# Kernel optimization log

Measured on AMD Instinct MI355X. Metric: run time of the kernel, lower is better.

The kernel has to match this reference:

```python
import jax, jax.numpy as jnp
import numpy as np

PI = float(np.pi)


def _layernorm(x, g, b, eps=1e-5):
    mu = jnp.mean(x, axis=-1, keepdims=True)
    var = jnp.var(x, axis=-1, keepdims=True)
    return (x - mu) * jax.lax.rsqrt(var + eps) * g + b


def setup_inputs() -> dict:
    key = jax.random.key(0)
    B, L, D, P = 4, 2048, 256, 32
    ks = jax.random.split(key, 16)

    def lin_w(k, fi, fo):
        return (jax.random.normal(k, (fi, fo), dtype=jnp.float32) / np.sqrt(fi)).astype(jnp.float32)

    inp = {
        'x': jax.random.normal(ks[0], (B, L, D), dtype=jnp.float32),
        'pos_phases': jax.random.normal(ks[1], (L, P), dtype=jnp.float32) * PI,
        'w_mem1v': lin_w(ks[2], D, P), 'b_mem1v': jnp.zeros((P,), jnp.float32),
        'w_mem1o': lin_w(ks[3], P, D), 'b_mem1o': jnp.zeros((D,), jnp.float32),
        'w_off': lin_w(ks[4], D + P, P), 'b_off': jnp.zeros((P,), jnp.float32),
        'w_key': lin_w(ks[5], D, P), 'b_key': jnp.zeros((P,), jnp.float32),
        'w_val': lin_w(ks[6], D, D), 'b_val': jnp.zeros((D,), jnp.float32),
        'w_sk1': lin_w(ks[7], 2 * D, D), 'b_sk1': jnp.zeros((D,), jnp.float32),
        'w_sk2': lin_w(ks[8], D, P), 'b_sk2': jnp.zeros((P,), jnp.float32),
        'w_gate': lin_w(ks[9], D, 1), 'b_gate': jnp.zeros((1,), jnp.float32),
        'ln_g': jnp.ones((D,), jnp.float32), 'ln_b': jnp.zeros((D,), jnp.float32),
        'w_out': lin_w(ks[10], D, D), 'b_out': jnp.zeros((D,), jnp.float32),
    }
    return inp


def reference(x, pos_phases, w_mem1v, b_mem1v, w_mem1o, b_mem1o, w_off, b_off,
              w_key, b_key, w_val, b_val, w_sk1, b_sk1, w_sk2, b_sk2,
              w_gate, b_gate, ln_g, ln_b, w_out, b_out):
    B, L, D = x.shape
    P = pos_phases.shape[-1]

    pos_cos = jnp.cos(pos_phases)  # [L,P]
    pos_sin = jnp.sin(pos_phases)

    # Memory 1: flat [B,L,P] phasor cumulative memory
    v1 = x @ w_mem1v + b_mem1v                       # [B,L,P]
    mem1_cos = jnp.cumsum(pos_cos[None] * v1, axis=1)
    mem1_sin = jnp.cumsum(pos_sin[None] * v1, axis=1)

    offset_input = jnp.concatenate([x, jnp.broadcast_to(pos_phases[None], (B, L, P))], axis=-1)
    offset = jnp.tanh(offset_input @ w_off + b_off) * PI
    oc, os = jnp.cos(offset), jnp.sin(offset)
    query_cos = pos_cos[None] * oc - pos_sin[None] * os
    query_sin = pos_sin[None] * oc + pos_cos[None] * os
    pos_ret = (mem1_cos * query_cos + mem1_sin * query_sin) / np.sqrt(P)
    pos_out = pos_ret @ w_mem1o + b_mem1o            # [B,L,D]

    # Memory 2: full [B,L,P,D] phasor KV cumulative memory
    key_phases = jnp.tanh(x @ w_key + b_key) * PI    # [B,L,P]
    key_cos, key_sin = jnp.cos(key_phases), jnp.sin(key_phases)
    values = x @ w_val + b_val                       # [B,L,D]
    store_gate = jax.nn.sigmoid(x @ w_gate + b_gate) # [B,L,1]

    positions = jnp.arange(1, L + 1, dtype=x.dtype)[None, :, None]
    context_avg = jnp.cumsum(x, axis=1) / positions
    h = jax.nn.gelu(jnp.concatenate([x, context_avg], axis=-1) @ w_sk1 + b_sk1, approximate=False)
    storage_phases = jnp.tanh(h @ w_sk2 + b_sk2) * PI  # [B,L,P]

    gated_v = values * store_gate                    # [B,L,D]
    kv_mem_cos = jnp.cumsum(jnp.cos(storage_phases)[..., None] * gated_v[:, :, None, :], axis=1)  # [B,L,P,D]
    kv_mem_sin = jnp.cumsum(jnp.sin(storage_phases)[..., None] * gated_v[:, :, None, :], axis=1)

    gate_cumsum = jnp.clip(jnp.cumsum(store_gate, axis=1), 1.0, None)  # [B,L,1]
    kv_retrieved = jnp.einsum('blpd,blp->bld', kv_mem_cos, key_cos) + \
                   jnp.einsum('blpd,blp->bld', kv_mem_sin, key_sin)
    kv_retrieved = kv_retrieved / (jnp.sqrt(gate_cumsum) * np.sqrt(P))

    combined = pos_out + kv_retrieved
    return x + _layernorm(combined, ln_g, ln_b) @ w_out + b_out
```

## Files before the change

### kernel.cpp

```cpp
#include <hip/hip_runtime.h>
#include <hip/hip_bf16.h>

constexpr int B_ = 4;
constexpr int L_ = 2048;
constexpr int D_ = 256;
constexpr int P_ = 32;
constexpr int CL = 32;
constexpr int NC = L_ / CL;

#define PI_F 3.14159265358979323846f
#define INV_SQRT_P 0.17677669529663687f

typedef __attribute__((ext_vector_type(8))) short short8_t;
typedef __attribute__((ext_vector_type(4))) float floatx4;

static __device__ inline short f2bf(float f) {
  unsigned int u;
  __builtin_memcpy(&u, &f, 4);
  unsigned int r = (u + 0x7fffu + ((u >> 16) & 1u)) >> 16;
  return (short)r;
}
static __device__ inline float bf2f(short s) {
  unsigned int u = ((unsigned int)(unsigned short)s) << 16;
  float f;
  __builtin_memcpy(&f, &u, 4);
  return f;
}

__global__ void wprep(const float* __restrict__ x, const float* __restrict__ pos,
                      const float* __restrict__ w_val, const float* __restrict__ w_mem1v,
                      const float* __restrict__ w_off, const float* __restrict__ b_off,
                      const float* __restrict__ w_key, const float* __restrict__ w_gate,
                      const float* __restrict__ w_sk1, const float* __restrict__ w_out,
                      const float* __restrict__ w_sk2, const float* __restrict__ w_mem1o,
                      short* __restrict__ WA, short* __restrict__ W1,
                      short* __restrict__ WO, short* __restrict__ W2T,
                      short* __restrict__ W1OT,
                      short* __restrict__ xbf, float* __restrict__ poff) {
  int blk = blockIdx.x, tid = threadIdx.x;
  if (blk < 384) {
    int idx = blk * 256 + tid;
    int n = idx >> 8, k = idx & 255;
    float v;
    if (n < 256) v = w_val[k * 256 + n];
    else if (n < 288) v = w_mem1v[k * 32 + (n - 256)];
    else if (n < 320) v = w_off[k * 32 + (n - 288)];
    else if (n < 352) v = w_key[k * 32 + (n - 320)];
    else if (n == 352) v = w_gate[k];
    else v = 0.f;
    WA[idx] = f2bf(v);
  } else if (blk < 896) {
    int idx = (blk - 384) * 256 + tid;
    int n = idx >> 9, k = idx & 511;
    W1[idx] = f2bf(w_sk1[k * 256 + n]);
  } else if (blk < 1152) {
    int idx = (blk - 896) * 256 + tid;
    int n = idx >> 8, k = idx & 255;
    WO[idx] = f2bf(w_out[k * 256 + n]);
  } else if (blk < 1184) {
    int idx = (blk - 1152) * 256 + tid;
    int p = idx >> 8, k = idx & 255;
    W2T[idx] = f2bf(w_sk2[k * 32 + p]);
  } else if (blk < 1216) {
    int idx = (blk - 1184) * 256 + tid;
    int d = idx >> 5, p = idx & 31;
    W1OT[idx] = f2bf(w_mem1o[p * 256 + d]);
  } else if (blk < 3264) {
    int idx = ((blk - 1216) * 256 + tid) * 4;
    float4 v = *(const float4*)&x[idx];
    short4 o;
    o.x = f2bf(v.x); o.y = f2bf(v.y); o.z = f2bf(v.z); o.w = f2bf(v.w);
    *(short4*)&xbf[idx] = o;
  } else {
    int idx = (blk - 3264) * 256 + tid;
    int l = idx >> 5, p = idx & 31;
    float a = b_off[p];
    for (int j = 0; j < 32; ++j) a += pos[l * 32 + j] * w_off[(256 + j) * 32 + p];
    poff[idx] = a;
  }
}

template <int KTILES, int NBLK, int MODE>
__global__ __launch_bounds__(256) void gemm_k(const short* __restrict__ A0,
                                              const short* __restrict__ A1,
                                              const short* __restrict__ W,
                                              const float* __restrict__ bias,
                                              const float* __restrict__ xres,
                                              float* __restrict__ outf,
                                              short* __restrict__ outb) {
  __shared__ short As[64][136];
  __shared__ short Bs[64][136];
  int tid = threadIdx.x;
  int mg = blockIdx.x / NBLK, ng = blockIdx.x % NBLK;
  int tok0 = mg * 64, n0 = ng * 64;
  int lane = tid & 63, w = tid >> 6;
  int mw = (w & 1) * 32, nw = (w >> 1) * 32;
  floatx4 acc[2][2] = {{{0.f, 0.f, 0.f, 0.f}, {0.f, 0.f, 0.f, 0.f}},
                       {{0.f, 0.f, 0.f, 0.f}, {0.f, 0.f, 0.f, 0.f}}};
  int r2 = tid >> 4, c8 = tid & 15;
  int ml = lane & 15, kq = (lane >> 4) * 8;
  const int K = KTILES * 128;

  for (int kt = 0; kt < KTILES; ++kt) {
    const short* Asrc;
    int cb;
    if (KTILES == 4) {
      Asrc = (kt < 2) ? A0 : A1;
      cb = (kt & 1) * 128;
    } else {
      Asrc = A0;
      cb = kt * 128;
    }
#pragma unroll
    for (int pass = 0; pass < 4; ++pass) {
      int row = pass * 16 + r2;
      *(short8_t*)&As[row][c8 * 8] =
          *(const short8_t*)&Asrc[(tok0 + row) * 256 + cb + c8 * 8];
      *(short8_t*)&Bs[row][c8 * 8] =
          *(const short8_t*)&W[(n0 + row) * K + kt * 128 + c8 * 8];
    }
    __syncthreads();
#pragma unroll
    for (int s = 0; s < 4; ++s) {
      short8_t a0 = *(short8_t*)&As[mw + ml][s * 32 + kq];
      short8_t a1 = *(short8_t*)&As[mw + 16 + ml][s * 32 + kq];
      short8_t b0 = *(short8_t*)&Bs[nw + ml][s * 32 + kq];
      short8_t b1 = *(short8_t*)&Bs[nw + 16 + ml][s * 32 + kq];
      acc[0][0] = __builtin_amdgcn_mfma_f32_16x16x32_bf16(a0, b0, acc[0][0], 0, 0, 0);
      acc[0][1] = __builtin_amdgcn_mfma_f32_16x16x32_bf16(a0, b1, acc[0][1], 0, 0, 0);
      acc[1][0] = __builtin_amdgcn_mfma_f32_16x16x32_bf16(a1, b0, acc[1][0], 0, 0, 0);
      acc[1][1] = __builtin_amdgcn_mfma_f32_16x16x32_bf16(a1, b1, acc[1][1], 0, 0, 0);
    }
    __syncthreads();
  }
  int col = lane & 15, rq = (lane >> 4) * 4;
#pragma unroll
  for (int nt = 0; nt < 2; ++nt) {
    int n = n0 + nw + nt * 16 + col;
    float bv = (MODE == 0) ? 0.f : bias[n];
#pragma unroll
    for (int mt = 0; mt < 2; ++mt) {
#pragma unroll
      for (int rg = 0; rg < 4; ++rg) {
        int tok = tok0 + mw + mt * 16 + rq + rg;
        float v = acc[mt][nt][rg] + bv;
        if (MODE == 0) {
          outb[tok * 384 + n] = f2bf(v);
        } else if (MODE == 1) {
          float g = 0.5f * v * (1.f + erff(v * 0.70710678118654752f));
          outb[tok * 256 + n] = f2bf(g);
        } else {
          outf[tok * 256 + n] = xres[tok * 256 + n] + v;
        }
      }
    }
  }
}

__global__ void kernelA3(const short* __restrict__ Ybf, const float* __restrict__ pos,
                         const float* __restrict__ poff, const float* __restrict__ b_mem1v,
                         const float* __restrict__ b_key, const float* __restrict__ b_gate,
                         const float* __restrict__ b_val,
                         float* __restrict__ m1cT, float* __restrict__ m1sT,
                         float* __restrict__ qc, float* __restrict__ qs,
                         short* __restrict__ K2bf, short* __restrict__ gvT,
                         float* __restrict__ sg) {
  __shared__ float gsh[8];
  int tid = threadIdx.x;
  int tok0 = blockIdx.x * 8;
  int t = tid >> 5, p = tid & 31;
  int tok = tok0 + t, l = tok & (L_ - 1);
  int b = tok >> 11;
  float gate = 1.f / (1.f + expf(-(bf2f(Ybf[tok * 384 + 352]) + b_gate[0])));
  if (p == 0) {
    sg[tok] = gate;
    gsh[t] = gate;
  }
  float v1 = bf2f(Ybf[tok * 384 + 256 + p]) + b_mem1v[p];
  float ph = pos[l * 32 + p];
  float pc = cosf(ph), ps = sinf(ph);
  int idxT = (b * 32 + p) * L_ + l;
  m1cT[idxT] = pc * v1;
  m1sT[idxT] = ps * v1;
  float off = tanhf(bf2f(Ybf[tok * 384 + 288 + p]) + poff[l * 32 + p]) * PI_F;
  float oc = cosf(off), os = sinf(off);
  int idx = tok * 32 + p;
  qc[idx] = pc * oc - ps * os;
  qs[idx] = ps * oc + pc * os;
  float kp = tanhf(bf2f(Ybf[tok * 384 + 320 + p]) + b_key[p]) * PI_F;
  K2bf[tok * 64 + p] = f2bf(cosf(kp));
  K2bf[tok * 64 + 32 + p] = f2bf(sinf(kp));
  __syncthreads();
  {
    int l0 = tok0 & (L_ - 1);
    int bc = (tok0 >> 11) * NC + (l0 >> 5);
    int tl0 = l0 & 31;
    short sv[8];
#pragma unroll
    for (int tt = 0; tt < 8; ++tt)
      sv[tt] = f2bf((bf2f(Ybf[(tok0 + tt) * 384 + tid]) + b_val[tid]) * gsh[tt]);
    *(short8_t*)&gvT[(bc * 256 + tid) * 32 + tl0] = *(short8_t*)sv;
  }
}

__global__ void scan_all(float* __restrict__ m1cT, float* __restrict__ m1sT,
                         float* __restrict__ sg, const float* __restrict__ x,
                         float* __restrict__ ctxsum) {
  int blk = blockIdx.x;
  int tid = threadIdx.x;
  if (blk >= 260) {
    int c2 = blk - 260;
    int b = c2 >> 6, ch = c2 & 63;
    int xb = (b * L_ + ch * 32) * 256 + tid;
    float s = 0.f;
#pragma unroll 8
    for (int i = 0; i < 32; ++i) s += x[xb + i * 256];
    ctxsum[c2 * 256 + tid] = s;
    return;
  }
  int lane = tid & 63, wid = tid >> 6;
  __shared__ float wsum[4];
  float carry = 0.f;
  float* arr;
  int base;
  if (blk < 256) {
    arr = (blk < 128) ? m1cT : m1sT;
    base = (blk & 127) * L_;
  } else {
    arr = sg;
    base = (blk - 256) * L_;
  }
  for (int t0 = 0; t0 < L_; t0 += 256) {
    int l = t0 + tid;
    float v = arr[base + l];
#pragma unroll
    for (int off = 1; off < 64; off <<= 1) {
      float n = __shfl_up(v, off, 64);
      if (lane >= off) v += n;
    }
    if (lane == 63) wsum[wid] = v;
    __syncthreads();
    float add = carry;
    for (int w = 0; w < wid; ++w) add += wsum[w];
    arr[base + l] = v + add;
    carry += wsum[0] + wsum[1] + wsum[2] + wsum[3];
    __syncthreads();
  }
}

__global__ void kernelCtx(const float* __restrict__ x, const float* __restrict__ ctxsum,
                          short* __restrict__ ctxbf) {
  int c2 = blockIdx.x;
  int b = c2 >> 6, ch = c2 & 63;
  int tid = threadIdx.x;
  float run = 0.f;
  int sb = b * 64 * 256 + tid;
  for (int c = 0; c < ch; ++c) run += ctxsum[sb + c * 256];
  int xb = (b * L_ + ch * 32) * 256 + tid;
#pragma unroll 8
  for (int i = 0; i < 32; ++i) {
    run += x[xb + i * 256];
    int l = ch * 32 + i;
    ctxbf[xb + i * 256] = f2bf(run / (float)(l + 1));
  }
}

__global__ __launch_bounds__(256) void kernelCD(const short* __restrict__ hs,
                                                const short* __restrict__ W2T,
                                                const float* __restrict__ b_sk2,
                                                const short* __restrict__ gvT,
                                                short* __restrict__ SPbf,
                                                short* __restrict__ UT) {
  __shared__ __align__(16) short SPL[2][64][40];
  int tid = threadIdx.x;
  int tok0 = blockIdx.x * 64;
  int lane = tid & 63, w = tid >> 6;
  int ml = lane & 15, quad = lane >> 4, kq = quad * 8;
  int m0 = w * 16;
  floatx4 pacc[2] = {};
#pragma unroll
  for (int s = 0; s < 8; ++s) {
    short8_t a = *(const short8_t*)&hs[(tok0 + m0 + ml) * 256 + s * 32 + kq];
    short8_t b0 = *(const short8_t*)&W2T[ml * 256 + s * 32 + kq];
    short8_t b1 = *(const short8_t*)&W2T[(16 + ml) * 256 + s * 32 + kq];
    pacc[0] = __builtin_amdgcn_mfma_f32_16x16x32_bf16(a, b0, pacc[0], 0, 0, 0);
    pacc[1] = __builtin_amdgcn_mfma_f32_16x16x32_bf16(a, b1, pacc[1], 0, 0, 0);
  }
  int cl = w >> 1;
#pragma unroll
  for (int nt = 0; nt < 2; ++nt) {
    int p = nt * 16 + ml;
    float bs = b_sk2[p];
#pragma unroll
    for (int r = 0; r < 4; ++r) {
      int tok = tok0 + m0 + quad * 4 + r;
      float sp = tanhf(pacc[nt][r] + bs) * PI_F;
      short c = f2bf(cosf(sp)), s = f2bf(sinf(sp));
      int tl = (w & 1) * 16 + quad * 4 + r;
      SPL[cl][p][tl] = c;
      SPL[cl][32 + p][tl] = s;
      SPbf[tok * 64 + p] = c;
      SPbf[tok * 64 + 32 + p] = s;
    }
  }
  __syncthreads();
  int c2 = w & 1, dbase = (w >> 1) * 128;
  int bc = blockIdx.x * 2 + c2;
  short8_t a[4];
#pragma unroll
  for (int mt = 0; mt < 4; ++mt) a[mt] = *(short8_t*)&SPL[c2][mt * 16 + ml][kq];
#pragma unroll
  for (int dp = 0; dp < 2; ++dp) {
    floatx4 acc[4][4] = {};
#pragma unroll
    for (int nt = 0; nt < 4; ++nt) {
      short8_t b = *(const short8_t*)&gvT[(bc * 256 + dbase + dp * 64 + nt * 16 + ml) * 32 + kq];
#pragma unroll
      for (int mt = 0; mt < 4; ++mt)
        acc[mt][nt] = __builtin_amdgcn_mfma_f32_16x16x32_bf16(a[mt], b, acc[mt][nt], 0, 0, 0);
    }
#pragma unroll
    for (int mt = 0; mt < 4; ++mt)
#pragma unroll
      for (int nt = 0; nt < 4; ++nt)
#pragma unroll
        for (int r = 0; r < 4; ++r) {
          int q = mt * 16 + quad * 4 + r;
          int d = dbase + dp * 64 + nt * 16 + ml;
          UT[(bc * 256 + d) * 64 + q] = f2bf(acc[mt][nt][r]);
        }
  }
}

__global__ void kernelE(short* __restrict__ UT) {
  int tid = blockIdx.x * 256 + threadIdx.x;
  int q = tid & 63;
  int d = (tid >> 6) & 255;
  int b = tid >> 14;
  int base = ((b * NC) * 256 + d) * 64 + q;
  const int cs = 256 * 64;
  float run = 0.f;
  for (int c0 = 0; c0 < NC; c0 += 8) {
    short v[8];
#pragma unroll
    for (int j = 0; j < 8; ++j) v[j] = UT[base + (c0 + j) * cs];
#pragma unroll
    for (int j = 0; j < 8; ++j) {
      UT[base + (c0 + j) * cs] = f2bf(run);
      run += bf2f(v[j]);
    }
  }
}

__global__ __launch_bounds__(256) void kernelFG(const short* __restrict__ UT,
                                                const short* __restrict__ SPbf,
                                                const short* __restrict__ K2bf,
                                                const short* __restrict__ gvT,
                                                const float* __restrict__ sgc,
                                                const float* __restrict__ m1cT,
                                                const float* __restrict__ m1sT,
                                                const float* __restrict__ qc,
                                                const float* __restrict__ qs,
                                                const short* __restrict__ W1OT,
                                                const float* __restrict__ b_mem1o,
                                                const float* __restrict__ ln_g,
                                                const float* __restrict__ ln_b,
                                                short* __restrict__ cbn) {
  __shared__ __align__(16) short SL[32][40];
  __shared__ __align__(16) short PR[32][40];
  __shared__ float CMB[32][260];
  __shared__ float scl[32], mu_s[32], rs_s[32];
  int tid = threadIdx.x;
  int bc = blockIdx.x;
  int lbase = bc * CL;
  int bb = bc >> 6, lloc = (bc & 63) * 32;
  if (tid < 32) scl[tid] = rsqrtf(fmaxf(sgc[lbase + tid], 1.f)) * INV_SQRT_P;
  for (int it = 0; it < 4; ++it) {
    int i = it * 256 + tid;
    int p = i >> 5, t = i & 31;
    int gT = (bb * 32 + p) * L_ + lloc + t;
    int g = (lbase + t) * 32 + p;
    PR[t][p] = f2bf((m1cT[gT] * qc[g] + m1sT[gT] * qs[g]) * INV_SQRT_P);
  }
  int lane = tid & 63, w = tid >> 6;
  int ml = lane & 15, quad = lane >> 4, kq = quad * 8;
  floatx4 acc[2][4] = {};
  short8_t ka0 = *(const short8_t*)&K2bf[(lbase + ml) * 64 + kq];
  short8_t ka1 = *(const short8_t*)&K2bf[(lbase + 16 + ml) * 64 + kq];
  short8_t kb0 = *(const short8_t*)&K2bf[(lbase + ml) * 64 + 32 + kq];
  short8_t kb1 = *(const short8_t*)&K2bf[(lbase + 16 + ml) * 64 + 32 + kq];
#pragma unroll
  for (int nt = 0; nt < 4; ++nt) {
    short8_t b = *(const short8_t*)&UT[(bc * 256 + w * 64 + nt * 16 + ml) * 64 + kq];
    acc[0][nt] = __builtin_amdgcn_mfma_f32_16x16x32_bf16(ka0, b, acc[0][nt], 0, 0, 0);
    acc[1][nt] = __builtin_amdgcn_mfma_f32_16x16x32_bf16(ka1, b, acc[1][nt], 0, 0, 0);
  }
  if (w == 0) {
    floatx4 sacc[2][2] = {};
#pragma unroll
    for (int ks2 = 0; ks2 < 2; ++ks2) {
      short8_t a0 = (ks2 == 0) ? ka0 : kb0;
      short8_t a1 = (ks2 == 0) ? ka1 : kb1;
      short8_t b0 = *(const short8_t*)&SPbf[(lbase + ml) * 64 + ks2 * 32 + kq];
      short8_t b1 = *(const short8_t*)&SPbf[(lbase + 16 + ml) * 64 + ks2 * 32 + kq];
      sacc[0][0] = __builtin_amdgcn_mfma_f32_16x16x32_bf16(a0, b0, sacc[0][0], 0, 0, 0);
      sacc[0][1] = __builtin_amdgcn_mfma_f32_16x16x32_bf16(a0, b1, sacc[0][1], 0, 0, 0);
      sacc[1][0] = __builtin_amdgcn_mfma_f32_16x16x32_bf16(a1, b0, sacc[1][0], 0, 0, 0);
      sacc[1][1] = __builtin_amdgcn_mfma_f32_16x16x32_bf16(a1, b1, sacc[1][1], 0, 0, 0);
    }
#pragma unroll
    for (int mt = 0; mt < 2; ++mt)
#pragma unroll
      for (int nt = 0; nt < 2; ++nt)
#pragma unroll
        for (int r = 0; r < 4; ++r) {
          int trow = mt * 16 + quad * 4 + r;
          int scol = nt * 16 + ml;
          float v = (scol <= trow) ? sacc[mt][nt][r] : 0.f;
          SL[trow][scol] = f2bf(v);
        }
  }
  __syncthreads();
#pragma unroll
  for (int nt = 0; nt < 4; ++nt) {
    short8_t b = *(const short8_t*)&UT[(bc * 256 + w * 64 + nt * 16 + ml) * 64 + 32 + kq];
    acc[0][nt] = __builtin_amdgcn_mfma_f32_16x16x32_bf16(kb0, b, acc[0][nt], 0, 0, 0);
    acc[1][nt] = __builtin_amdgcn_mfma_f32_16x16x32_bf16(kb1, b, acc[1][nt], 0, 0, 0);
  }
  {
    short8_t a0 = *(short8_t*)&SL[ml][kq];
    short8_t a1 = *(short8_t*)&SL[16 + ml][kq];
#pragma unroll
    for (int nt = 0; nt < 4; ++nt) {
      short8_t b = *(const short8_t*)&gvT[(bc * 256 + w * 64 + nt * 16 + ml) * 32 + kq];
      acc[0][nt] = __builtin_amdgcn_mfma_f32_16x16x32_bf16(a0, b, acc[0][nt], 0, 0, 0);
      acc[1][nt] = __builtin_amdgcn_mfma_f32_16x16x32_bf16(a1, b, acc[1][nt], 0, 0, 0);
    }
  }
  floatx4 macc[2][4] = {};
  {
    short8_t a0 = *(short8_t*)&PR[ml][kq];
    short8_t a1 = *(short8_t*)&PR[16 + ml][kq];
#pragma unroll
    for (int nt = 0; nt < 4; ++nt) {
      short8_t b = *(const short8_t*)&W1OT[(w * 64 + nt * 16 + ml) * 32 + kq];
      macc[0][nt] = __builtin_amdgcn_mfma_f32_16x16x32_bf16(a0, b, macc[0][nt], 0, 0, 0);
      macc[1][nt] = __builtin_amdgcn_mfma_f32_16x16x32_bf16(a1, b, macc[1][nt], 0, 0, 0);
    }
  }
#pragma unroll
  for (int mt = 0; mt < 2; ++mt)
#pragma unroll
    for (int nt = 0; nt < 4; ++nt) {
      int d = w * 64 + nt * 16 + ml;
      float bm = b_mem1o[d];
#pragma unroll
      for (int r = 0; r < 4; ++r) {
        int t = mt * 16 + quad * 4 + r;
        CMB[t][d] = acc[mt][nt][r] * scl[t] + macc[mt][nt][r] + bm;
      }
    }
  __syncthreads();
  {
    int t = tid >> 3, g = tid & 7;
    float s = 0.f, s2 = 0.f;
#pragma unroll
    for (int j = 0; j < 32; ++j) {
      float v = CMB[t][g + j * 8];
      s += v;
      s2 += v * v;
    }
#pragma unroll
    for (int m = 1; m < 8; m <<= 1) {
      s += __shfl_xor(s, m, 64);
      s2 += __shfl_xor(s2, m, 64);
    }
    if (g == 0) {
      float mu = s / (float)D_;
      float var = s2 / (float)D_ - mu * mu;
      mu_s[t] = mu;
      rs_s[t] = rsqrtf(var + 1e-5f);
    }
  }
  __syncthreads();
  {
    float lg = ln_g[tid], lb = ln_b[tid];
#pragma unroll
    for (int t = 0; t < 32; ++t)
      cbn[(lbase + t) * 256 + tid] = f2bf((CMB[t][tid] - mu_s[t]) * rs_s[t] * lg + lb);
  }
}

extern "C" void kernel_launch(void* const* d_in, const int* in_sizes, int n_in,
                              void* d_out, int out_size, void* d_ws, size_t ws_size,
                              hipStream_t stream) {
  const float* x = (const float*)d_in[0];
  const float* pos = (const float*)d_in[1];
  const float* w_mem1v = (const float*)d_in[2];
  const float* b_mem1v = (const float*)d_in[3];
  const float* w_mem1o = (const float*)d_in[4];
  const float* b_mem1o = (const float*)d_in[5];
  const float* w_off = (const float*)d_in[6];
  const float* b_off = (const float*)d_in[7];
  const float* w_key = (const float*)d_in[8];
  const float* b_key = (const float*)d_in[9];
  const float* w_val = (const float*)d_in[10];
  const float* b_val = (const float*)d_in[11];
  const float* w_sk1 = (const float*)d_in[12];
  const float* b_sk1 = (const float*)d_in[13];
  const float* w_sk2 = (const float*)d_in[14];
  const float* b_sk2 = (const float*)d_in[15];
  const float* w_gate = (const float*)d_in[16];
  const float* b_gate = (const float*)d_in[17];
  const float* ln_g = (const float*)d_in[18];
  const float* ln_b = (const float*)d_in[19];
  const float* w_out = (const float*)d_in[20];
  const float* b_out = (const float*)d_in[21];
  float* out = (float*)d_out;
  float* ws = (float*)d_ws;

  const int BLP = B_ * L_ * P_;
  const int BLD = B_ * L_ * D_;
  float* m1cT = ws;
  float* m1sT = m1cT + BLP;
  float* qc = m1sT + BLP;
  float* qs = qc + BLP;
  float* sg = qs + BLP;
  float* poff = sg + B_ * L_;
  float* ctxsum = poff + L_ * P_;
  short* Ybf = (short*)(ctxsum + B_ * 64 * 256);
  short* UT = Ybf;
  short* xbf = UT + (size_t)B_ * NC * 256 * 64;
  short* cbn = xbf;
  short* ctxbf = xbf + BLD;
  short* hs = ctxbf + BLD;
  short* gvT = hs + BLD;
  short* K2bf = gvT + BLD;
  short* SPbf = K2bf + B_ * L_ * 64;
  short* WA = SPbf + B_ * L_ * 64;
  short* W1 = WA + 384 * 256;
  short* WO = W1 + 256 * 512;
  short* W2T = WO + 256 * 256;
  short* W1OT = W2T + 32 * 256;

  wprep<<<3520, 256, 0, stream>>>(x, pos, w_val, w_mem1v, w_off, b_off, w_key, w_gate,
                                  w_sk1, w_out, w_sk2, w_mem1o, WA, W1, WO, W2T, W1OT,
                                  xbf, poff);
  gemm_k<2, 6, 0><<<128 * 6, 256, 0, stream>>>(xbf, nullptr, WA, nullptr, nullptr, nullptr, Ybf);
  kernelA3<<<(B_ * L_) / 8, 256, 0, stream>>>(Ybf, pos, poff, b_mem1v, b_key, b_gate, b_val,
                                              m1cT, m1sT, qc, qs, K2bf, gvT, sg);
  scan_all<<<516, 256, 0, stream>>>(m1cT, m1sT, sg, x, ctxsum);
  kernelCtx<<<256, 256, 0, stream>>>(x, ctxsum, ctxbf);
  gemm_k<4, 4, 1><<<128 * 4, 256, 0, stream>>>(xbf, ctxbf, W1, b_sk1, nullptr, nullptr, hs);
  kernelCD<<<(B_ * L_) / 64, 256, 0, stream>>>(hs, W2T, b_sk2, gvT, SPbf, UT);
  kernelE<<<256, 256, 0, stream>>>(UT);
  kernelFG<<<B_ * NC, 256, 0, stream>>>(UT, SPbf, K2bf, gvT, sg, m1cT, m1sT, qc, qs,
                                        W1OT, b_mem1o, ln_g, ln_b, cbn);
  gemm_k<2, 4, 2><<<128 * 4, 256, 0, stream>>>(cbn, nullptr, WO, b_out, x, out, nullptr);
}
```

Baseline: 190.6 us.

## Fuse scan-stage kernels into persistent launches with software grid barriers

Merges kernelA3, scan_all and kernelCtx into one 516-block kernel, and kernelCD, kernelE and kernelFG into one 256-block kernel. The stages are separated by atomic-counter grid barriers instead of kernel boundaries. This removes several launch gaps and tail drains. It relies on every block being co-resident, which risks deadlock if occupancy is not enough, and it adds barrier latency. kernelA3 now handles 16 tokens per block instead of 8.

```diff
diff --git a/kernel.cpp b/kernel.cpp
--- a/kernel.cpp
+++ b/kernel.cpp
@@ -25,6 +25,24 @@
   float f;
   __builtin_memcpy(&f, &u, 4);
   return f;
+}
+
+static __device__ inline void gbar(unsigned* bar, unsigned nb) {
+  __syncthreads();
+  if (threadIdx.x == 0) {
+    __threadfence();
+    unsigned g = __hip_atomic_load(bar + 1, __ATOMIC_ACQUIRE, __HIP_MEMORY_SCOPE_AGENT);
+    unsigned a = __hip_atomic_fetch_add(bar, 1u, __ATOMIC_ACQ_REL, __HIP_MEMORY_SCOPE_AGENT);
+    if (a + 1 == nb) {
+      __hip_atomic_store(bar, 0u, __ATOMIC_RELAXED, __HIP_MEMORY_SCOPE_AGENT);
+      __hip_atomic_fetch_add(bar + 1, 1u, __ATOMIC_RELEASE, __HIP_MEMORY_SCOPE_AGENT);
+    } else {
+      while (__hip_atomic_load(bar + 1, __ATOMIC_ACQUIRE, __HIP_MEMORY_SCOPE_AGENT) == g)
+        __builtin_amdgcn_s_sleep(2);
+    }
+    __threadfence();
+  }
+  __syncthreads();
 }
 
 __global__ void wprep(const float* __restrict__ x, const float* __restrict__ pos,
@@ -36,8 +54,10 @@
                       short* __restrict__ WA, short* __restrict__ W1,
                       short* __restrict__ WO, short* __restrict__ W2T,
                       short* __restrict__ W1OT,
-                      short* __restrict__ xbf, float* __restrict__ poff) {
+                      short* __restrict__ xbf, float* __restrict__ poff,
+                      unsigned* __restrict__ bar) {
   int blk = blockIdx.x, tid = threadIdx.x;
+  if (blk == 0 && tid < 8) bar[tid] = 0u;
   if (blk < 384) {
     int idx = blk * 256 + tid;
     int n = idx >> 8, k = idx & 255;
@@ -157,57 +177,62 @@
   }
 }
 
-__global__ void kernelA3(const short* __restrict__ Ybf, const float* __restrict__ pos,
-                         const float* __restrict__ poff, const float* __restrict__ b_mem1v,
-                         const float* __restrict__ b_key, const float* __restrict__ b_gate,
-                         const float* __restrict__ b_val,
-                         float* __restrict__ m1cT, float* __restrict__ m1sT,
-                         float* __restrict__ qc, float* __restrict__ qs,
-                         short* __restrict__ K2bf, short* __restrict__ gvT,
-                         float* __restrict__ sg) {
-  __shared__ float gsh[8];
-  int tid = threadIdx.x;
-  int tok0 = blockIdx.x * 8;
-  int t = tid >> 5, p = tid & 31;
-  int tok = tok0 + t, l = tok & (L_ - 1);
-  int b = tok >> 11;
-  float gate = 1.f / (1.f + expf(-(bf2f(Ybf[tok * 384 + 352]) + b_gate[0])));
-  if (p == 0) {
-    sg[tok] = gate;
-    gsh[t] = gate;
-  }
-  float v1 = bf2f(Ybf[tok * 384 + 256 + p]) + b_mem1v[p];
-  float ph = pos[l * 32 + p];
-  float pc = cosf(ph), ps = sinf(ph);
-  int idxT = (b * 32 + p) * L_ + l;
-  m1cT[idxT] = pc * v1;
-  m1sT[idxT] = ps * v1;
-  float off = tanhf(bf2f(Ybf[tok * 384 + 288 + p]) + poff[l * 32 + p]) * PI_F;
-  float oc = cosf(off), os = sinf(off);
-  int idx = tok * 32 + p;
-  qc[idx] = pc * oc - ps * os;
-  qs[idx] = ps * oc + pc * os;
-  float kp = tanhf(bf2f(Ybf[tok * 384 + 320 + p]) + b_key[p]) * PI_F;
-  K2bf[tok * 64 + p] = f2bf(cosf(kp));
-  K2bf[tok * 64 + 32 + p] = f2bf(sinf(kp));
-  __syncthreads();
-  {
-    int l0 = tok0 & (L_ - 1);
-    int bc = (tok0 >> 11) * NC + (l0 >> 5);
-    int tl0 = l0 & 31;
-    short sv[8];
-#pragma unroll
-    for (int tt = 0; tt < 8; ++tt)
-      sv[tt] = f2bf((bf2f(Ybf[(tok0 + tt) * 384 + tid]) + b_val[tid]) * gsh[tt]);
-    *(short8_t*)&gvT[(bc * 256 + tid) * 32 + tl0] = *(short8_t*)sv;
-  }
-}
-
-__global__ void scan_all(float* __restrict__ m1cT, float* __restrict__ m1sT,
-                         float* __restrict__ sg, const float* __restrict__ x,
-                         float* __restrict__ ctxsum) {
-  int blk = blockIdx.x;
-  int tid = threadIdx.x;
+__global__ __launch_bounds__(256, 4) void kernelA3SC(
+    const short* __restrict__ Ybf, const float* __restrict__ pos,
+    const float* __restrict__ poff, const float* __restrict__ b_mem1v,
+    const float* __restrict__ b_key, const float* __restrict__ b_gate,
+    const float* __restrict__ b_val,
+    float* __restrict__ m1cT, float* __restrict__ m1sT,
+    float* __restrict__ qc, float* __restrict__ qs,
+    short* __restrict__ K2bf, short* __restrict__ gvT,
+    float* __restrict__ sg, const float* __restrict__ x,
+    float* __restrict__ ctxsum, short* __restrict__ ctxbf,
+    unsigned* __restrict__ bar) {
+  __shared__ float gsh[16];
+  __shared__ float wsum[4];
+  int blk = blockIdx.x, tid = threadIdx.x;
+  if (blk < 512) {
+    int tok0 = blk * 16;
+#pragma unroll
+    for (int h = 0; h < 2; ++h) {
+      int t = h * 8 + (tid >> 5), p = tid & 31;
+      int tok = tok0 + t, l = tok & (L_ - 1);
+      int b = tok >> 11;
+      float gate = 1.f / (1.f + expf(-(bf2f(Ybf[tok * 384 + 352]) + b_gate[0])));
+      if (p == 0) {
+        sg[tok] = gate;
+        gsh[t] = gate;
+      }
+      float v1 = bf2f(Ybf[tok * 384 + 256 + p]) + b_mem1v[p];
+      float ph = pos[l * 32 + p];
+      float pc = cosf(ph), ps = sinf(ph);
+      int idxT = (b * 32 + p) * L_ + l;
+      m1cT[idxT] = pc * v1;
+      m1sT[idxT] = ps * v1;
+      float off = tanhf(bf2f(Ybf[tok * 384 + 288 + p]) + poff[l * 32 + p]) * PI_F;
+      float oc = cosf(off), os = sinf(off);
+      int idx = tok * 32 + p;
+      qc[idx] = pc * oc - ps * os;
+      qs[idx] = ps * oc + pc * os;
+      float kp = tanhf(bf2f(Ybf[tok * 384 + 320 + p]) + b_key[p]) * PI_F;
+      K2bf[tok * 64 + p] = f2bf(cosf(kp));
+      K2bf[tok * 64 + 32 + p] = f2bf(sinf(kp));
+    }
+    __syncthreads();
+    {
+      int l0 = tok0 & (L_ - 1);
+      int bc = (tok0 >> 11) * NC + (l0 >> 5);
+      int tl0 = l0 & 31;
+      short sv[16];
+#pragma unroll
+      for (int tt = 0; tt < 16; ++tt)
+        sv[tt] = f2bf((bf2f(Ybf[(tok0 + tt) * 384 + tid]) + b_val[tid]) * gsh[tt]);
+      int gb = (bc * 256 + tid) * 32 + tl0;
+      *(short8_t*)&gvT[gb] = *(short8_t*)&sv[0];
+      *(short8_t*)&gvT[gb + 8] = *(short8_t*)&sv[8];
+    }
+  }
+  gbar(bar + 0, gridDim.x);
   if (blk >= 260) {
     int c2 = blk - 260;
     int b = c2 >> 6, ch = c2 & 63;
@@ -216,278 +241,270 @@
 #pragma unroll 8
     for (int i = 0; i < 32; ++i) s += x[xb + i * 256];
     ctxsum[c2 * 256 + tid] = s;
-    return;
-  }
-  int lane = tid & 63, wid = tid >> 6;
-  __shared__ float wsum[4];
-  float carry = 0.f;
-  float* arr;
-  int base;
-  if (blk < 256) {
-    arr = (blk < 128) ? m1cT : m1sT;
-    base = (blk & 127) * L_;
   } else {
-    arr = sg;
-    base = (blk - 256) * L_;
-  }
-  for (int t0 = 0; t0 < L_; t0 += 256) {
-    int l = t0 + tid;
-    float v = arr[base + l];
-#pragma unroll
-    for (int off = 1; off < 64; off <<= 1) {
-      float n = __shfl_up(v, off, 64);
-      if (lane >= off) v += n;
-    }
-    if (lane == 63) wsum[wid] = v;
-    __syncthreads();
-    float add = carry;
-    for (int w = 0; w < wid; ++w) add += wsum[w];
-    arr[base + l] = v + add;
-    carry += wsum[0] + wsum[1] + wsum[2] + wsum[3];
-    __syncthreads();
-  }
-}
-
-__global__ void kernelCtx(const float* __restrict__ x, const float* __restrict__ ctxsum,
-                          short* __restrict__ ctxbf) {
-  int c2 = blockIdx.x;
-  int b = c2 >> 6, ch = c2 & 63;
-  int tid = threadIdx.x;
-  float run = 0.f;
-  int sb = b * 64 * 256 + tid;
-  for (int c = 0; c < ch; ++c) run += ctxsum[sb + c * 256];
-  int xb = (b * L_ + ch * 32) * 256 + tid;
+    int lane = tid & 63, wid = tid >> 6;
+    float carry = 0.f;
+    float* arr;
+    int base;
+    if (blk < 256) {
+      arr = (blk < 128) ? m1cT : m1sT;
+      base = (blk & 127) * L_;
+    } else {
+      arr = sg;
+      base = (blk - 256) * L_;
+    }
+    for (int t0 = 0; t0 < L_; t0 += 256) {
+      int l = t0 + tid;
+      float v = arr[base + l];
+#pragma unroll
+      for (int off = 1; off < 64; off <<= 1) {
+        float n = __shfl_up(v, off, 64);
+        if (lane >= off) v += n;
+      }
+      if (lane == 63) wsum[wid] = v;
+      __syncthreads();
+      float add = carry;
+      for (int w = 0; w < wid; ++w) add += wsum[w];
+      arr[base + l] = v + add;
+      carry += wsum[0] + wsum[1] + wsum[2] + wsum[3];
+      __syncthreads();
+    }
+  }
+  gbar(bar + 2, gridDim.x);
+  if (blk >= 260) {
+    int c2 = blk - 260;
+    int b = c2 >> 6, ch = c2 & 63;
+    float run = 0.f;
+    int sb = b * 64 * 256 + tid;
+    for (int c = 0; c < ch; ++c) run += ctxsum[sb + c * 256];
+    int xb = (b * L_ + ch * 32) * 256 + tid;
 #pragma unroll 8
-  for (int i = 0; i < 32; ++i) {
-    run += x[xb + i * 256];
-    int l = ch * 32 + i;
-    ctxbf[xb + i * 256] = f2bf(run / (float)(l + 1));
-  }
-}
-
-__global__ __launch_bounds__(256) void kernelCD(const short* __restrict__ hs,
-                                                const short* __restrict__ W2T,
-                                                const float* __restrict__ b_sk2,
-                                                const short* __restrict__ gvT,
-                                                short* __restrict__ SPbf,
-                                                short* __restrict__ UT) {
-  __shared__ __align__(16) short SPL[2][64][40];
-  int tid = threadIdx.x;
-  int tok0 = blockIdx.x * 64;
+    for (int i = 0; i < 32; ++i) {
+      run += x[xb + i * 256];
+      int l = ch * 32 + i;
+      ctxbf[xb + i * 256] = f2bf(run / (float)(l + 1));
+    }
+  }
+}
+
+__global__ __launch_bounds__(256) void kernelKV(
+    const short* __restrict__ hs, const short* __restrict__ W2T,
+    const float* __restrict__ b_sk2, const short* __restrict__ gvT,
+    short* __restrict__ SPbf, short* __restrict__ UT,
+    const short* __restrict__ K2bf, const float* __restrict__ sgc,
+    const float* __restrict__ m1cT, const float* __restrict__ m1sT,
+    const float* __restrict__ qc, const float* __restrict__ qs,
+    const short* __restrict__ W1OT, const float* __restrict__ b_mem1o,
+    const float* __restrict__ ln_g, const float* __restrict__ ln_b,
+    short* __restrict__ cbn, unsigned* __restrict__ bar) {
+  __shared__ __align__(16) char shm[38912];
+  int blk = blockIdx.x, tid = threadIdx.x;
   int lane = tid & 63, w = tid >> 6;
   int ml = lane & 15, quad = lane >> 4, kq = quad * 8;
-  int m0 = w * 16;
-  floatx4 pacc[2] = {};
-#pragma unroll
-  for (int s = 0; s < 8; ++s) {
-    short8_t a = *(const short8_t*)&hs[(tok0 + m0 + ml) * 256 + s * 32 + kq];
-    short8_t b0 = *(const short8_t*)&W2T[ml * 256 + s * 32 + kq];
-    short8_t b1 = *(const short8_t*)&W2T[(16 + ml) * 256 + s * 32 + kq];
-    pacc[0] = __builtin_amdgcn_mfma_f32_16x16x32_bf16(a, b0, pacc[0], 0, 0, 0);
-    pacc[1] = __builtin_amdgcn_mfma_f32_16x16x32_bf16(a, b1, pacc[1], 0, 0, 0);
-  }
-  int cl = w >> 1;
-#pragma unroll
-  for (int nt = 0; nt < 2; ++nt) {
-    int p = nt * 16 + ml;
-    float bs = b_sk2[p];
-#pragma unroll
-    for (int r = 0; r < 4; ++r) {
-      int tok = tok0 + m0 + quad * 4 + r;
-      float sp = tanhf(pacc[nt][r] + bs) * PI_F;
-      short c = f2bf(cosf(sp)), s = f2bf(sinf(sp));
-      int tl = (w & 1) * 16 + quad * 4 + r;
-      SPL[cl][p][tl] = c;
-      SPL[cl][32 + p][tl] = s;
-      SPbf[tok * 64 + p] = c;
-      SPbf[tok * 64 + 32 + p] = s;
-    }
-  }
-  __syncthreads();
-  int c2 = w & 1, dbase = (w >> 1) * 128;
-  int bc = blockIdx.x * 2 + c2;
-  short8_t a[4];
-#pragma unroll
-  for (int mt = 0; mt < 4; ++mt) a[mt] = *(short8_t*)&SPL[c2][mt * 16 + ml][kq];
-#pragma unroll
-  for (int dp = 0; dp < 2; ++dp) {
-    floatx4 acc[4][4] = {};
+  if (blk < 128) {
+    short* SPL = (short*)shm;
+    int tok0 = blk * 64;
+    int m0 = w * 16;
+    floatx4 pacc[2] = {};
+#pragma unroll
+    for (int s = 0; s < 8; ++s) {
+      short8_t a = *(const short8_t*)&hs[(tok0 + m0 + ml) * 256 + s * 32 + kq];
+      short8_t b0 = *(const short8_t*)&W2T[ml * 256 + s * 32 + kq];
+      short8_t b1 = *(const short8_t*)&W2T[(16 + ml) * 256 + s * 32 + kq];
+      pacc[0] = __builtin_amdgcn_mfma_f32_16x16x32_bf16(a, b0, pacc[0], 0, 0, 0);
+      pacc[1] = __builtin_amdgcn_mfma_f32_16x16x32_bf16(a, b1, pacc[1], 0, 0, 0);
+    }
+    int cl = w >> 1;
+#pragma unroll
+    for (int nt = 0; nt < 2; ++nt) {
+      int p = nt * 16 + ml;
+      float bs = b_sk2[p];
+#pragma unroll
+      for (int r = 0; r < 4; ++r) {
+        int tok = tok0 + m0 + quad * 4 + r;
+        float sp = tanhf(pacc[nt][r] + bs) * PI_F;
+        short c = f2bf(cosf(sp)), s = f2bf(sinf(sp));
+        int tl = (w & 1) * 16 + quad * 4 + r;
+        SPL[(cl * 64 + p) * 40 + tl] = c;
+        SPL[(cl * 64 + 32 + p) * 40 + tl] = s;
+        SPbf[tok * 64 + p] = c;
+        SPbf[tok * 64 + 32 + p] = s;
+      }
+    }
+    __syncthreads();
+    int c2 = w & 1, dbase = (w >> 1) * 128;
+    int bc = blk * 2 + c2;
+    short8_t a[4];
+#pragma unroll
+    for (int mt = 0; mt < 4; ++mt)
+      a[mt] = *(short8_t*)&SPL[(c2 * 64 + mt * 16 + ml) * 40 + kq];
+#pragma unroll
+    for (int dp = 0; dp < 2; ++dp) {
+      floatx4 acc[4][4] = {};
+#pragma unroll
+      for (int nt = 0; nt < 4; ++nt) {
+        short8_t b = *(const short8_t*)&gvT[(bc * 256 + dbase + dp * 64 + nt * 16 + ml) * 32 + kq];
+#pragma unroll
+        for (int mt = 0; mt < 4; ++mt)
+          acc[mt][nt] = __builtin_amdgcn_mfma_f32_16x16x32_bf16(a[mt], b, acc[mt][nt], 0, 0, 0);
+      }
+#pragma unroll
+      for (int mt = 0; mt < 4; ++mt)
+#pragma unroll
+        for (int nt = 0; nt < 4; ++nt)
+#pragma unroll
+          for (int r = 0; r < 4; ++r) {
+            int q = mt * 16 + quad * 4 + r;
+            int d = dbase + dp * 64 + nt * 16 + ml;
+            UT[(bc * 256 + d) * 64 + q] = f2bf(acc[mt][nt][r]);
+          }
+    }
+  }
+  gbar(bar + 4, gridDim.x);
+  {
+    int gt = blk * 256 + tid;
+    int q = gt & 63;
+    int d = (gt >> 6) & 255;
+    int b = gt >> 14;
+    int base = ((b * NC) * 256 + d) * 64 + q;
+    const int cs = 256 * 64;
+    float run = 0.f;
+    for (int c0 = 0; c0 < NC; c0 += 8) {
+      short v[8];
+#pragma unroll
+      for (int j = 0; j < 8; ++j) v[j] = UT[base + (c0 + j) * cs];
+#pragma unroll
+      for (int j = 0; j < 8; ++j) {
+        UT[base + (c0 + j) * cs] = f2bf(run);
+        run += bf2f(v[j]);
+      }
+    }
+  }
+  gbar(bar + 6, gridDim.x);
+  {
+    short* SL = (short*)shm;
+    short* PR = SL + 32 * 40;
+    float* CMB = (float*)(shm + 5120);
+    float* scl = (float*)(shm + 5120 + 33280);
+    float* mu_s = scl + 32;
+    float* rs_s = scl + 64;
+    int bc = blk;
+    int lbase = bc * CL;
+    int bb = bc >> 6, lloc = (bc & 63) * 32;
+    if (tid < 32) scl[tid] = rsqrtf(fmaxf(sgc[lbase + tid], 1.f)) * INV_SQRT_P;
+    for (int it = 0; it < 4; ++it) {
+      int i = it * 256 + tid;
+      int p = i >> 5, t = i & 31;
+      int gT = (bb * 32 + p) * L_ + lloc + t;
+      int g = (lbase + t) * 32 + p;
+      PR[t * 40 + p] = f2bf((m1cT[gT] * qc[g] + m1sT[gT] * qs[g]) * INV_SQRT_P);
+    }
+    floatx4 acc[2][4] = {};
+    short8_t ka0 = *(const short8_t*)&K2bf[(lbase + ml) * 64 + kq];
+    short8_t ka1 = *(const short8_t*)&K2bf[(lbase + 16 + ml) * 64 + kq];
+    short8_t kb0 = *(const short8_t*)&K2bf[(lbase + ml) * 64 + 32 + kq];
+    short8_t kb1 = *(const short8_t*)&K2bf[(lbase + 16 + ml) * 64 + 32 + kq];
 #pragma unroll
     for (int nt = 0; nt < 4; ++nt) {
-      short8_t b = *(const short8_t*)&gvT[(bc * 256 + dbase + dp * 64 + nt * 16 + ml) * 32 + kq];
-#pragma unroll
-      for (int mt = 0; mt < 4; ++mt)
-        acc[mt][nt] = __builtin_amdgcn_mfma_f32_16x16x32_bf16(a[mt], b, acc[mt][nt], 0, 0, 0);
-    }
-#pragma unroll
-    for (int mt = 0; mt < 4; ++mt)
-#pragma unroll
-      for (int nt = 0; nt < 4; ++nt)
+      short8_t b = *(const short8_t*)&UT[(bc * 256 + w * 64 + nt * 16 + ml) * 64 + kq];
+      acc[0][nt] = __builtin_amdgcn_mfma_f32_16x16x32_bf16(ka0, b, acc[0][nt], 0, 0, 0);
+      acc[1][nt] = __builtin_amdgcn_mfma_f32_16x16x32_bf16(ka1, b, acc[1][nt], 0, 0, 0);
+    }
+    if (w == 0) {
+      floatx4 sacc[2][2] = {};
+#pragma unroll
+      for (int ks2 = 0; ks2 < 2; ++ks2) {
+        short8_t a0 = (ks2 == 0) ? ka0 : kb0;
+        short8_t a1 = (ks2 == 0) ? ka1 : kb1;
+        short8_t b0 = *(const short8_t*)&SPbf[(lbase + ml) * 64 + ks2 * 32 + kq];
+        short8_t b1 = *(const short8_t*)&SPbf[(lbase + 16 + ml) * 64 + ks2 * 32 + kq];
+        sacc[0][0] = __builtin_amdgcn_mfma_f32_16x16x32_bf16(a0, b0, sacc[0][0], 0, 0, 0);
+        sacc[0][1] = __builtin_amdgcn_mfma_f32_16x16x32_bf16(a0, b1, sacc[0][1], 0, 0, 0);
+        sacc[1][0] = __builtin_amdgcn_mfma_f32_16x16x32_bf16(a1, b0, sacc[1][0], 0, 0, 0);
+        sacc[1][1] = __builtin_amdgcn_mfma_f32_16x16x32_bf16(a1, b1, sacc[1][1], 0, 0, 0);
+      }
+#pragma unroll
+      for (int mt = 0; mt < 2; ++mt)
+#pragma unroll
+        for (int nt = 0; nt < 2; ++nt)
+#pragma unroll
+          for (int r = 0; r < 4; ++r) {
+            int trow = mt * 16 + quad * 4 + r;
+            int scol = nt * 16 + ml;
+            float v = (scol <= trow) ? sacc[mt][nt][r] : 0.f;
+            SL[trow * 40 + scol] = f2bf(v);
+          }
+    }
+    __syncthreads();
+#pragma unroll
+    for (int nt = 0; nt < 4; ++nt) {
+      short8_t b = *(const short8_t*)&UT[(bc * 256 + w * 64 + nt * 16 + ml) * 64 + 32 + kq];
+      acc[0][nt] = __builtin_amdgcn_mfma_f32_16x16x32_bf16(kb0, b, acc[0][nt], 0, 0, 0);
+      acc[1][nt] = __builtin_amdgcn_mfma_f32_16x16x32_bf16(kb1, b, acc[1][nt], 0, 0, 0);
+    }
+    {
+      short8_t a0 = *(short8_t*)&SL[ml * 40 + kq];
+      short8_t a1 = *(short8_t*)&SL[(16 + ml) * 40 + kq];
+#pragma unroll
+      for (int nt = 0; nt < 4; ++nt) {
+        short8_t b = *(const short8_t*)&gvT[(bc * 256 + w * 64 + nt * 16 + ml) * 32 + kq];
+        acc[0][nt] = __builtin_amdgcn_mfma_f32_16x16x32_bf16(a0, b, acc[0][nt], 0, 0, 0);
+        acc[1][nt] = __builtin_amdgcn_mfma_f32_16x16x32_bf16(a1, b, acc[1][nt], 0, 0, 0);
+      }
+    }
+    floatx4 macc[2][4] = {};
+    {
+      short8_t a0 = *(short8_t*)&PR[ml * 40 + kq];
+      short8_t a1 = *(short8_t*)&PR[(16 + ml) * 40 + kq];
+#pragma unroll
+      for (int nt = 0; nt < 4; ++nt) {
+        short8_t b = *(const short8_t*)&W1OT[(w * 64 + nt * 16 + ml) * 32 + kq];
+        macc[0][nt] = __builtin_amdgcn_mfma_f32_16x16x32_bf16(a0, b, macc[0][nt], 0, 0, 0);
+        macc[1][nt] = __builtin_amdgcn_mfma_f32_16x16x32_bf16(a1, b, macc[1][nt], 0, 0, 0);
+      }
+    }
+#pragma unroll
+    for (int mt = 0; mt < 2; ++mt)
+#pragma unroll
+      for (int nt = 0; nt < 4; ++nt) {
+        int d = w * 64 + nt * 16 + ml;
+        float bm = b_mem1o[d];
 #pragma unroll
         for (int r = 0; r < 4; ++r) {
-          int q = mt * 16 + quad * 4 + r;
-          int d = dbase + dp * 64 + nt * 16 + ml;
-          UT[(bc * 256 + d) * 64 + q] = f2bf(acc[mt][nt][r]);
+          int t = mt * 16 + quad * 4 + r;
+          CMB[t * 260 + d] = acc[mt][nt][r] * scl[t] + macc[mt][nt][r] + bm;
         }
-  }
-}
-
-__global__ void kernelE(short* __restrict__ UT) {
-  int tid = blockIdx.x * 256 + threadIdx.x;
-  int q = tid & 63;
-  int d = (tid >> 6) & 255;
-  int b = tid >> 14;
-  int base = ((b * NC) * 256 + d) * 64 + q;
-  const int cs = 256 * 64;
-  float run = 0.f;
-  for (int c0 = 0; c0 < NC; c0 += 8) {
-    short v[8];
-#pragma unroll
-    for (int j = 0; j < 8; ++j) v[j] = UT[base + (c0 + j) * cs];
-#pragma unroll
-    for (int j = 0; j < 8; ++j) {
-      UT[base + (c0 + j) * cs] = f2bf(run);
-      run += bf2f(v[j]);
-    }
-  }
-}
-
-__global__ __launch_bounds__(256) void kernelFG(const short* __restrict__ UT,
-                                                const short* __restrict__ SPbf,
-                                                const short* __restrict__ K2bf,
-                                                const short* __restrict__ gvT,
-                                                const float* __restrict__ sgc,
-                                                const float* __restrict__ m1cT,
-                                                const float* __restrict__ m1sT,
-                                                const float* __restrict__ qc,
-                                                const float* __restrict__ qs,
-                                                const short* __restrict__ W1OT,
-                                                const float* __restrict__ b_mem1o,
-                                                const float* __restrict__ ln_g,
-                                                const float* __restrict__ ln_b,
-                                                short* __restrict__ cbn) {
-  __shared__ __align__(16) short SL[32][40];
-  __shared__ __align__(16) short PR[32][40];
-  __shared__ float CMB[32][260];
-  __shared__ float scl[32], mu_s[32], rs_s[32];
-  int tid = threadIdx.x;
-  int bc = blockIdx.x;
-  int lbase = bc * CL;
-  int bb = bc >> 6, lloc = (bc & 63) * 32;
-  if (tid < 32) scl[tid] = rsqrtf(fmaxf(sgc[lbase + tid], 1.f)) * INV_SQRT_P;
-  for (int it = 0; it < 4; ++it) {
-    int i = it * 256 + tid;
-    int p = i >> 5, t = i & 31;
-    int gT = (bb * 32 + p) * L_ + lloc + t;
-    int g = (lbase + t) * 32 + p;
-    PR[t][p] = f2bf((m1cT[gT] * qc[g] + m1sT[gT] * qs[g]) * INV_SQRT_P);
-  }
-  int lane = tid & 63, w = tid >> 6;
-  int ml = lane & 15, quad = lane >> 4, kq = quad * 8;
-  floatx4 acc[2][4] = {};
-  short8_t ka0 = *(const short8_t*)&K2bf[(lbase + ml) * 64 + kq];
-  short8_t ka1 = *(const short8_t*)&K2bf[(lbase + 16 + ml) * 64 + kq];
-  short8_t kb0 = *(const short8_t*)&K2bf[(lbase + ml) * 64 + 32 + kq];
-  short8_t kb1 = *(const short8_t*)&K2bf[(lbase + 16 + ml) * 64 + 32 + kq];
-#pragma unroll
-  for (int nt = 0; nt < 4; ++nt) {
-    short8_t b = *(const short8_t*)&UT[(bc * 256 + w * 64 + nt * 16 + ml) * 64 + kq];
-    acc[0][nt] = __builtin_amdgcn_mfma_f32_16x16x32_bf16(ka0, b, acc[0][nt], 0, 0, 0);
-    acc[1][nt] = __builtin_amdgcn_mfma_f32_16x16x32_bf16(ka1, b, acc[1][nt], 0, 0, 0);
-  }
-  if (w == 0) {
-    floatx4 sacc[2][2] = {};
-#pragma unroll
-    for (int ks2 = 0; ks2 < 2; ++ks2) {
-      short8_t a0 = (ks2 == 0) ? ka0 : kb0;
-      short8_t a1 = (ks2 == 0) ? ka1 : kb1;
-      short8_t b0 = *(const short8_t*)&SPbf[(lbase + ml) * 64 + ks2 * 32 + kq];
-      short8_t b1 = *(const short8_t*)&SPbf[(lbase + 16 + ml) * 64 + ks2 * 32 + kq];
-      sacc[0][0] = __builtin_amdgcn_mfma_f32_16x16x32_bf16(a0, b0, sacc[0][0], 0, 0, 0);
-      sacc[0][1] = __builtin_amdgcn_mfma_f32_16x16x32_bf16(a0, b1, sacc[0][1], 0, 0, 0);
-      sacc[1][0] = __builtin_amdgcn_mfma_f32_16x16x32_bf16(a1, b0, sacc[1][0], 0, 0, 0);
-      sacc[1][1] = __builtin_amdgcn_mfma_f32_16x16x32_bf16(a1, b1, sacc[1][1], 0, 0, 0);
-    }
-#pragma unroll
-    for (int mt = 0; mt < 2; ++mt)
-#pragma unroll
-      for (int nt = 0; nt < 2; ++nt)
-#pragma unroll
-        for (int r = 0; r < 4; ++r) {
-          int trow = mt * 16 + quad * 4 + r;
-          int scol = nt * 16 + ml;
-          float v = (scol <= trow) ? sacc[mt][nt][r] : 0.f;
-          SL[trow][scol] = f2bf(v);
-        }
-  }
-  __syncthreads();
-#pragma unroll
-  for (int nt = 0; nt < 4; ++nt) {
-    short8_t b = *(const short8_t*)&UT[(bc * 256 + w * 64 + nt * 16 + ml) * 64 + 32 + kq];
-    acc[0][nt] = __builtin_amdgcn_mfma_f32_16x16x32_bf16(kb0, b, acc[0][nt], 0, 0, 0);
-    acc[1][nt] = __builtin_amdgcn_mfma_f32_16x16x32_bf16(kb1, b, acc[1][nt], 0, 0, 0);
-  }
-  {
-    short8_t a0 = *(short8_t*)&SL[ml][kq];
-    short8_t a1 = *(short8_t*)&SL[16 + ml][kq];
-#pragma unroll
-    for (int nt = 0; nt < 4; ++nt) {
-      short8_t b = *(const short8_t*)&gvT[(bc * 256 + w * 64 + nt * 16 + ml) * 32 + kq];
-      acc[0][nt] = __builtin_amdgcn_mfma_f32_16x16x32_bf16(a0, b, acc[0][nt], 0, 0, 0);
-      acc[1][nt] = __builtin_amdgcn_mfma_f32_16x16x32_bf16(a1, b, acc[1][nt], 0, 0, 0);
-    }
-  }
-  floatx4 macc[2][4] = {};
-  {
-    short8_t a0 = *(short8_t*)&PR[ml][kq];
-    short8_t a1 = *(short8_t*)&PR[16 + ml][kq];
-#pragma unroll
-    for (int nt = 0; nt < 4; ++nt) {
-      short8_t b = *(const short8_t*)&W1OT[(w * 64 + nt * 16 + ml) * 32 + kq];
-      macc[0][nt] = __builtin_amdgcn_mfma_f32_16x16x32_bf16(a0, b, macc[0][nt], 0, 0, 0);
-      macc[1][nt] = __builtin_amdgcn_mfma_f32_16x16x32_bf16(a1, b, macc[1][nt], 0, 0, 0);
-    }
-  }
-#pragma unroll
-  for (int mt = 0; mt < 2; ++mt)
-#pragma unroll
-    for (int nt = 0; nt < 4; ++nt) {
-      int d = w * 64 + nt * 16 + ml;
-      float bm = b_mem1o[d];
-#pragma unroll
-      for (int r = 0; r < 4; ++r) {
-        int t = mt * 16 + quad * 4 + r;
-        CMB[t][d] = acc[mt][nt][r] * scl[t] + macc[mt][nt][r] + bm;
-      }
-    }
-  __syncthreads();
-  {
-    int t = tid >> 3, g = tid & 7;
-    float s = 0.f, s2 = 0.f;
-#pragma unroll
-    for (int j = 0; j < 32; ++j) {
-      float v = CMB[t][g + j * 8];
-      s += v;
-      s2 += v * v;
-    }
-#pragma unroll
-    for (int m = 1; m < 8; m <<= 1) {
-      s += __shfl_xor(s, m, 64);
-      s2 += __shfl_xor(s2, m, 64);
-    }
-    if (g == 0) {
-      float mu = s / (float)D_;
-      float var = s2 / (float)D_ - mu * mu;
-      mu_s[t] = mu;
-      rs_s[t] = rsqrtf(var + 1e-5f);
-    }
-  }
-  __syncthreads();
-  {
-    float lg = ln_g[tid], lb = ln_b[tid];
-#pragma unroll
-    for (int t = 0; t < 32; ++t)
-      cbn[(lbase + t) * 256 + tid] = f2bf((CMB[t][tid] - mu_s[t]) * rs_s[t] * lg + lb);
+      }
+    __syncthreads();
+    {
+      int t = tid >> 3, g = tid & 7;
+      float s = 0.f, s2 = 0.f;
+#pragma unroll
+      for (int j = 0; j < 32; ++j) {
+        float v = CMB[t * 260 + g + j * 8];
+        s += v;
+        s2 += v * v;
+      }
+#pragma unroll
+      for (int m = 1; m < 8; m <<= 1) {
+        s += __shfl_xor(s, m, 64);
+        s2 += __shfl_xor(s2, m, 64);
+      }
+      if (g == 0) {
+        float mu = s / (float)D_;
+        float var = s2 / (float)D_ - mu * mu;
+        mu_s[t] = mu;
+        rs_s[t] = rsqrtf(var + 1e-5f);
+      }
+    }
+    __syncthreads();
+    {
+      float lg = ln_g[tid], lb = ln_b[tid];
+#pragma unroll
+      for (int t = 0; t < 32; ++t)
+        cbn[(lbase + t) * 256 + tid] =
+            f2bf((CMB[t * 260 + tid] - mu_s[t]) * rs_s[t] * lg + lb);
+    }
   }
 }
 
@@ -542,19 +559,18 @@
   short* WO = W1 + 256 * 512;
   short* W2T = WO + 256 * 256;
   short* W1OT = W2T + 32 * 256;
+  unsigned* bar = (unsigned*)(W1OT + 256 * 32);
 
   wprep<<<3520, 256, 0, stream>>>(x, pos, w_val, w_mem1v, w_off, b_off, w_key, w_gate,
                                   w_sk1, w_out, w_sk2, w_mem1o, WA, W1, WO, W2T, W1OT,
-                                  xbf, poff);
+                                  xbf, poff, bar);
   gemm_k<2, 6, 0><<<128 * 6, 256, 0, stream>>>(xbf, nullptr, WA, nullptr, nullptr, nullptr, Ybf);
-  kernelA3<<<(B_ * L_) / 8, 256, 0, stream>>>(Ybf, pos, poff, b_mem1v, b_key, b_gate, b_val,
-                                              m1cT, m1sT, qc, qs, K2bf, gvT, sg);
-  scan_all<<<516, 256, 0, stream>>>(m1cT, m1sT, sg, x, ctxsum);
-  kernelCtx<<<256, 256, 0, stream>>>(x, ctxsum, ctxbf);
+  kernelA3SC<<<516, 256, 0, stream>>>(Ybf, pos, poff, b_mem1v, b_key, b_gate, b_val,
+                                      m1cT, m1sT, qc, qs, K2bf, gvT, sg, x, ctxsum,
+                                      ctxbf, bar);
   gemm_k<4, 4, 1><<<128 * 4, 256, 0, stream>>>(xbf, ctxbf, W1, b_sk1, nullptr, nullptr, hs);
-  kernelCD<<<(B_ * L_) / 64, 256, 0, stream>>>(hs, W2T, b_sk2, gvT, SPbf, UT);
-  kernelE<<<256, 256, 0, stream>>>(UT);
-  kernelFG<<<B_ * NC, 256, 0, stream>>>(UT, SPbf, K2bf, gvT, sg, m1cT, m1sT, qc, qs,
-                                        W1OT, b_mem1o, ln_g, ln_b, cbn);
+  kernelKV<<<256, 256, 0, stream>>>(hs, W2T, b_sk2, gvT, SPbf, UT, K2bf, sg,
+                                    m1cT, m1sT, qc, qs, W1OT, b_mem1o, ln_g, ln_b,
+                                    cbn, bar);
   gemm_k<2, 4, 2><<<128 * 4, 256, 0, stream>>>(cbn, nullptr, WO, b_out, x, out, nullptr);
 }
```

Result: slower. 443.9 us (+133.0%).
